# Kernel optimization log

Measured on AMD Instinct MI355X. Metric: run time of the kernel, lower is better.

The kernel has to match this reference:

```python
import jax, jax.numpy as jnp
import numpy as np

S = 64            # rendered_size
CLASS_NUM = 14    # dataset.enc_len
NEG_SLOPE = 0.01
EPS = 1e-5


def _conv(x, w, stride, pad):
    return jax.lax.conv_general_dilated(
        x, w, (stride, stride), [(pad, pad), (pad, pad)],
        dimension_numbers=("NCHW", "OIHW", "NCHW"))


def _bn(x, gamma, beta):
    # BatchNorm2d in training mode: biased batch stats over (N,H,W)
    m = jnp.mean(x, axis=(0, 2, 3), keepdims=True)
    v = jnp.var(x, axis=(0, 2, 3), keepdims=True)
    xn = (x - m) * jax.lax.rsqrt(v + EPS)
    return xn * gamma.reshape(1, -1, 1, 1) + beta.reshape(1, -1, 1, 1)


def _lrelu(x):
    return jnp.where(x >= 0, x, NEG_SLOPE * x)


def _render(elements):
    # elements: (B, N, class_num+4)
    rects = elements[:, :, -4:]
    cls = elements[:, :, :-4]                       # (B, N, C)
    x = rects[:, :, 0][:, :, None, None] * S        # (B, N, 1, 1)
    y = rects[:, :, 1][:, :, None, None] * S
    w = rects[:, :, 2][:, :, None, None] * S
    h = rects[:, :, 3][:, :, None, None] * S
    x0, x1 = x - 0.5 * w, x + 0.5 * w
    y0, y1 = y - 0.5 * h, y + 0.5 * h
    cx = jnp.arange(S, dtype=elements.dtype)[None, None, None, :]  # varies along W
    cy = jnp.arange(S, dtype=elements.dtype)[None, None, :, None]  # varies along H
    k = lambda c, cr: jnp.maximum(1.0 - jnp.abs(c - cr), 0.0)
    b0 = lambda c, cr: jnp.clip(c - cr, 0.0, 1.0)
    b1 = lambda cr, c: jnp.clip(cr - c, 0.0, 1.0)
    by = b0(cy, y0) * b1(y1, cy)                    # (B, N, S, S)
    bx = b0(cx, x0) * b1(x1, cx)
    l0 = k(cx, x0) * by
    l1 = k(cx, x1) * by
    l2 = k(cy, y0) * bx
    l3 = k(cy, y1) * bx
    rendered = jnp.maximum(jnp.maximum(l0, l1), jnp.maximum(l2, l3))  # (B,N,S,S)
    # sum over elements of class one-hot * rendered -> (B, C, S, S)
    return jnp.einsum("bnc,bnhw->bchw", cls, rendered)


def setup_inputs() -> dict:
    key = jax.random.key(0)
    ks = jax.random.split(key, 8)
    B, N = 64, 46
    inp = {
        "input_data": jax.random.uniform(ks[0], (B, N, CLASS_NUM + 4), dtype=jnp.float32),
        "input_length": jax.random.randint(ks[1], (B,), 0, N, dtype=jnp.int32),
        # cnn convs (bias=False) + BN affine params
        "w1": jax.random.normal(ks[2], (64, CLASS_NUM, 5, 5), jnp.float32) * 0.05,
        "g1": jnp.ones((64,), jnp.float32), "b1": jnp.zeros((64,), jnp.float32),
        "w2": jax.random.normal(ks[3], (128, 64, 5, 5), jnp.float32) * 0.03,
        "g2": jnp.ones((128,), jnp.float32), "b2": jnp.zeros((128,), jnp.float32),
        "w3": jax.random.normal(ks[4], (256, 128, 5, 5), jnp.float32) * 0.02,
        "g3": jnp.ones((256,), jnp.float32), "b3": jnp.zeros((256,), jnp.float32),
        # classifier: conv k=8 (bias=False) + BN + 1x1 conv (bias=True)
        "w4": jax.random.normal(ks[5], (1024, 256, 8, 8), jnp.float32) * 0.01,
        "g4": jnp.ones((1024,), jnp.float32), "b4": jnp.zeros((1024,), jnp.float32),
        "w5": jax.random.normal(ks[6], (1, 1024, 1, 1), jnp.float32) * 0.03,
        "b5": jnp.zeros((1,), jnp.float32),
    }
    return inp


def reference(input_data, input_length, w1, g1, b1, w2, g2, b2,
              w3, g3, b3, w4, g4, b4, w5, b5):
    rendered = _render(input_data)                       # (B, C, 64, 64)
    h = _lrelu(_bn(_conv(rendered, w1, 2, 2), g1, b1))   # (B, 64, 32, 32)
    h = _lrelu(_bn(_conv(h, w2, 2, 2), g2, b2))          # (B, 128, 16, 16)
    h = _lrelu(_bn(_conv(h, w3, 2, 2), g3, b3))          # (B, 256, 8, 8)
    h = _lrelu(_bn(_conv(h, w4, 1, 0), g4, b4))          # (B, 1024, 1, 1)
    out = _conv(h, w5, 1, 0) + b5.reshape(1, -1, 1, 1)   # (B, 1, 1, 1)
    return out.squeeze()                                 # (B,)
```

## Files before the change

### kernel.cpp

```cpp
#include <hip/hip_runtime.h>
#include <hip/hip_bf16.h>

#define NEG 0.01f
#define EPS 1e-5f

typedef __attribute__((ext_vector_type(8))) short short8;
typedef __attribute__((ext_vector_type(4))) float floatx4;

__device__ inline unsigned short f2bf(float f) {
    __hip_bfloat16 h = __float2bfloat16(f);
    union { __hip_bfloat16 h; unsigned short u; } cv; cv.h = h;
    return cv.u;
}

__global__ __launch_bounds__(256) void render_kernel(const float* __restrict__ in,
                                                     unsigned short* __restrict__ out) {
    int b = blockIdx.x >> 4;
    int chunk = blockIdx.x & 15;
    __shared__ float r0[46], r1[46], r2[46], r3[46];
    __shared__ float cls_s[46 * 14];
    int tid = threadIdx.x;
    if (tid < 46) {
        const float* p = in + ((size_t)b * 46 + tid) * 18 + 14;
        float x = p[0] * 64.f, y = p[1] * 64.f, w = p[2] * 64.f, h = p[3] * 64.f;
        r0[tid] = x - 0.5f * w; r1[tid] = x + 0.5f * w;
        r2[tid] = y - 0.5f * h; r3[tid] = y + 0.5f * h;
    }
    for (int idx = tid; idx < 46 * 14; idx += 256) {
        int n = idx / 14, c = idx % 14;
        cls_s[idx] = in[((size_t)b * 46 + n) * 18 + c];
    }
    __syncthreads();
    if (tid < 33) {
        int j = chunk * 33 + tid;
        if (j < 528) {
            int y, x;
            if (j < 136) { y = j / 68; x = j - y * 68; }
            else if (j < 272) { int t = j - 136; int yy = t / 68; y = 66 + yy; x = t - yy * 68; }
            else { int t = j - 272; y = 2 + (t >> 2); int k = t & 3; x = (k < 2) ? k : 64 + k; }
            size_t zb = (((size_t)b * 68 + y) * 68 + x) * 16;
            short8 z;
#pragma unroll
            for (int i = 0; i < 8; ++i) z[i] = 0;
            *(short8*)(out + zb) = z;
            *(short8*)(out + zb + 8) = z;
        }
    }
    int pix = chunk * 256 + tid;
    float cx = (float)(pix & 63);
    float cy = (float)(pix >> 6);
    float acc[14];
#pragma unroll
    for (int c = 0; c < 14; ++c) acc[c] = 0.f;
    for (int n = 0; n < 46; ++n) {
        float x0 = r0[n], x1 = r1[n], y0 = r2[n], y1 = r3[n];
        float by = fminf(fmaxf(cy - y0, 0.f), 1.f) * fminf(fmaxf(y1 - cy, 0.f), 1.f);
        float bx = fminf(fmaxf(cx - x0, 0.f), 1.f) * fminf(fmaxf(x1 - cx, 0.f), 1.f);
        float kx0 = fmaxf(1.f - fabsf(cx - x0), 0.f);
        float kx1 = fmaxf(1.f - fabsf(cx - x1), 0.f);
        float ky0 = fmaxf(1.f - fabsf(cy - y0), 0.f);
        float ky1 = fmaxf(1.f - fabsf(cy - y1), 0.f);
        float r = fmaxf(fmaxf(kx0 * by, kx1 * by), fmaxf(ky0 * bx, ky1 * bx));
        if (r > 0.f) {
#pragma unroll
            for (int c = 0; c < 14; ++c) acc[c] = fmaf(cls_s[n * 14 + c], r, acc[c]);
        }
    }
    size_t obase = (((size_t)b * 68 + ((pix >> 6) + 2)) * 68 + ((pix & 63) + 2)) * 16;
    short8 v0, v1;
#pragma unroll
    for (int i = 0; i < 8; ++i) v0[i] = (short)f2bf(acc[i]);
#pragma unroll
    for (int i = 0; i < 6; ++i) v1[i] = (short)f2bf(acc[8 + i]);
    v1[6] = 0; v1[7] = 0;
    *(short8*)(out + obase) = v0;
    *(short8*)(out + obase + 8) = v1;
}

__global__ __launch_bounds__(256) void wtrans_all(const float* __restrict__ w1,
                                                  const float* __restrict__ w2,
                                                  const float* __restrict__ w3,
                                                  unsigned short* __restrict__ wT1,
                                                  unsigned short* __restrict__ wT2,
                                                  unsigned short* __restrict__ wT3) {
    int idx = blockIdx.x * 256 + threadIdx.x;
    const float* w; unsigned short* wT; int CIN, CPLOG, SUB, COLOG;
    if (idx < 30720) { w = w1; wT = wT1; CIN = 14; CPLOG = 4; SUB = 3; COLOG = 6; }
    else if (idx < 235520) { idx -= 30720; w = w2; wT = wT2; CIN = 64; CPLOG = 6; SUB = 10; COLOG = 7; }
    else if (idx < 1054720) { idx -= 235520; w = w3; wT = wT3; CIN = 128; CPLOG = 7; SUB = 20; COLOG = 8; }
    else return;
    int kk = idx & 31;
    int co = (idx >> 5) & ((1 << COLOG) - 1);
    int s = idx >> (5 + COLOG);
    int kh = s / SUB, sub = s - kh * SUB;
    int kidx = sub * 32 + kk;
    int kw = kidx >> CPLOG;
    int ci = kidx & ((1 << CPLOG) - 1);
    float v = (kw < 5 && ci < CIN) ? w[((size_t)(co * CIN + ci) * 5 + kh) * 5 + kw] : 0.f;
    wT[idx] = f2bf(v);
}

template <int CP, int COUT, int HP, int LOG_OHW, int LOG_OW, int SUB,
          int NCO, int NT, int CH, int NW>
__global__ __launch_bounds__(NW * 64) void conv_mfma(
        const unsigned short* __restrict__ inP,
        const unsigned short* __restrict__ wT,
        float* __restrict__ outX,
        float* __restrict__ stacc) {
    constexpr int NSTEP = 5 * SUB;
    constexpr int NCHUNK = NSTEP / CH;
    constexpr int COT = NT * 16;
    constexpr int NSV = CH * COT * 4;
    constexpr int NSTG = (NSV + NW * 64 - 1) / (NW * 64);
    static_assert(NSTEP % CH == 0, "CH must divide NSTEP");
    __shared__ short Bs[2][CH][COT][32];
    __shared__ float sred[NW][2][COT];
    int tid = threadIdx.x;
    int wave = tid >> 6, lane = tid & 63, q = lane >> 4, l16 = lane & 15;
    int cpx = gridDim.x >> 3;
    int lb = (blockIdx.x & 7) * cpx + (blockIdx.x >> 3);
    int bm = lb / NCO, bco = lb % NCO;

    const short* aB[4];
#pragma unroll
    for (int f = 0; f < 4; ++f) {
        int m = bm * (NW * 64) + wave * 64 + f * 16 + l16;
        int b = m >> LOG_OHW;
        int ohw = m & ((1 << LOG_OHW) - 1);
        int oh = ohw >> LOG_OW, ow = ohw & ((1 << LOG_OW) - 1);
        aB[f] = (const short*)inP + ((size_t)((b * HP + 2 * oh) * HP + 2 * ow)) * CP + q * 8;
    }
    const short* bgbase = (const short*)wT + (size_t)bco * COT * 32;

    floatx4 acc[4][NT];
#pragma unroll
    for (int f = 0; f < 4; ++f)
#pragma unroll
        for (int nt = 0; nt < NT; ++nt) acc[f][nt] = (floatx4){0.f, 0.f, 0.f, 0.f};

    short8 nb[NSTG];
#pragma unroll
    for (int i = 0; i < NSTG; ++i) {
        int v = tid + i * NW * 64;
        if (v < NSV) {
            int s = v / (COT * 4);
            int rem = v - s * (COT * 4);
            nb[i] = *(const short8*)(bgbase + ((size_t)s * COUT) * 32 + rem * 8);
        }
    }
#pragma unroll
    for (int i = 0; i < NSTG; ++i) {
        int v = tid + i * NW * 64;
        if (v < NSV) {
            int s = v / (COT * 4);
            int rem = v - s * (COT * 4);
            *(short8*)((short*)&Bs[0][s][0][0] + rem * 8) = nb[i];
        }
    }
    short8 afc[4], afn[4];
#pragma unroll
    for (int f = 0; f < 4; ++f) afc[f] = *(const short8*)(aB[f]);
    __syncthreads();

    for (int chunk = 0; chunk < NCHUNK; ++chunk) {
        int cur = chunk & 1;
        if (chunk + 1 < NCHUNK) {
            int step0 = (chunk + 1) * CH;
#pragma unroll
            for (int i = 0; i < NSTG; ++i) {
                int v = tid + i * NW * 64;
                if (v < NSV) {
                    int s = v / (COT * 4);
                    int rem = v - s * (COT * 4);
                    nb[i] = *(const short8*)(bgbase + ((size_t)(step0 + s) * COUT) * 32 + rem * 8);
                }
            }
        }
#pragma unroll
        for (int s = 0; s < CH; ++s) {
            int step = chunk * CH + s;
            int stepn = step + 1;
            if (stepn < NSTEP) {
                int khn = stepn / SUB, subn = stepn - khn * SUB;
#pragma unroll
                for (int f = 0; f < 4; ++f)
                    afn[f] = *(const short8*)(aB[f] + (size_t)(khn * HP) * CP + subn * 32);
            }
#pragma unroll
            for (int nt = 0; nt < NT; ++nt) {
                short8 bf = *(const short8*)&Bs[cur][s][nt * 16 + l16][q * 8];
#pragma unroll
                for (int f = 0; f < 4; ++f)
                    acc[f][nt] = __builtin_amdgcn_mfma_f32_16x16x32_bf16(afc[f], bf, acc[f][nt], 0, 0, 0);
            }
#pragma unroll
            for (int f = 0; f < 4; ++f) afc[f] = afn[f];
        }
        if (chunk + 1 < NCHUNK) {
#pragma unroll
            for (int i = 0; i < NSTG; ++i) {
                int v = tid + i * NW * 64;
                if (v < NSV) {
                    int s = v / (COT * 4);
                    int rem = v - s * (COT * 4);
                    *(short8*)((short*)&Bs[cur ^ 1][s][0][0] + rem * 8) = nb[i];
                }
            }
            __syncthreads();
        }
    }
#pragma unroll
    for (int f = 0; f < 4; ++f)
#pragma unroll
        for (int nt = 0; nt < NT; ++nt)
#pragma unroll
            for (int rg = 0; rg < 4; ++rg) {
                int mg = bm * (NW * 64) + wave * 64 + f * 16 + q * 4 + rg;
                int co = bco * COT + nt * 16 + l16;
                outX[(size_t)mg * COUT + co] = acc[f][nt][rg];
            }
#pragma unroll
    for (int nt = 0; nt < NT; ++nt) {
        float s = 0.f, s2 = 0.f;
#pragma unroll
        for (int f = 0; f < 4; ++f)
#pragma unroll
            for (int rg = 0; rg < 4; ++rg) {
                float v = acc[f][nt][rg];
                s += v; s2 = fmaf(v, v, s2);
            }
        s += __shfl_xor(s, 16); s += __shfl_xor(s, 32);
        s2 += __shfl_xor(s2, 16); s2 += __shfl_xor(s2, 32);
        if (q == 0) {
            sred[wave][0][nt * 16 + l16] = s;
            sred[wave][1][nt * 16 + l16] = s2;
        }
    }
    __syncthreads();
    if (tid < COT) {
        float ts = 0.f, ts2 = 0.f;
#pragma unroll
        for (int w = 0; w < NW; ++w) { ts += sred[w][0][tid]; ts2 += sred[w][1][tid]; }
        atomicAdd(&stacc[bco * COT + tid], ts);
        atomicAdd(&stacc[COUT + bco * COT + tid], ts2);
    }
}

__global__ __launch_bounds__(256) void conv4_mfma(const unsigned short* __restrict__ A,
                                                  const float* __restrict__ w4,
                                                  float* __restrict__ h4) {
    constexpr int CH = 4, NCHUNK = 8;
    __shared__ short Bs[CH][64][40];
    int tid = threadIdx.x;
    int bco = blockIdx.x & 15;
    int ks = blockIdx.x >> 4;
    int wave = tid >> 6, lane = tid & 63, q = lane >> 4, l16 = lane & 15;
    const short* aBase = (const short*)A + (size_t)(wave * 16 + l16) * 16384 + ks * 1024 + q * 8;
    int r = tid >> 2, cc = tid & 3;
    const float* bg = w4 + (size_t)(bco * 64 + r) * 16384 + ks * 1024 + cc * 8;

    floatx4 acc[4];
#pragma unroll
    for (int nt = 0; nt < 4; ++nt) acc[nt] = (floatx4){0.f, 0.f, 0.f, 0.f};

    short8 nb[CH];
#pragma unroll
    for (int s = 0; s < CH; ++s) {
        float4 b0 = *(const float4*)(bg + s * 32);
        float4 b1 = *(const float4*)(bg + s * 32 + 4);
        nb[s][0] = (short)f2bf(b0.x); nb[s][1] = (short)f2bf(b0.y);
        nb[s][2] = (short)f2bf(b0.z); nb[s][3] = (short)f2bf(b0.w);
        nb[s][4] = (short)f2bf(b1.x); nb[s][5] = (short)f2bf(b1.y);
        nb[s][6] = (short)f2bf(b1.z); nb[s][7] = (short)f2bf(b1.w);
    }
#pragma unroll
    for (int s = 0; s < CH; ++s) *(short8*)&Bs[s][r][cc * 8] = nb[s];
    __syncthreads();

    for (int chunk = 0; chunk < NCHUNK; ++chunk) {
        bool has_next = (chunk + 1 < NCHUNK);
        if (has_next) {
#pragma unroll
            for (int s = 0; s < CH; ++s) {
                int step = (chunk + 1) * CH + s;
                float4 b0 = *(const float4*)(bg + step * 32);
                float4 b1 = *(const float4*)(bg + step * 32 + 4);
                nb[s][0] = (short)f2bf(b0.x); nb[s][1] = (short)f2bf(b0.y);
                nb[s][2] = (short)f2bf(b0.z); nb[s][3] = (short)f2bf(b0.w);
                nb[s][4] = (short)f2bf(b1.x); nb[s][5] = (short)f2bf(b1.y);
                nb[s][6] = (short)f2bf(b1.z); nb[s][7] = (short)f2bf(b1.w);
            }
        }
#pragma unroll
        for (int s = 0; s < CH; ++s) {
            int step = chunk * CH + s;
            short8 af = *(const short8*)(aBase + step * 32);
#pragma unroll
            for (int nt = 0; nt < 4; ++nt) {
                short8 bf = *(const short8*)&Bs[s][nt * 16 + l16][q * 8];
                acc[nt] = __builtin_amdgcn_mfma_f32_16x16x32_bf16(af, bf, acc[nt], 0, 0, 0);
            }
        }
        if (has_next) {
            __syncthreads();
#pragma unroll
            for (int s = 0; s < CH; ++s) *(short8*)&Bs[s][r][cc * 8] = nb[s];
            __syncthreads();
        }
    }
#pragma unroll
    for (int nt = 0; nt < 4; ++nt) {
#pragma unroll
        for (int rg = 0; rg < 4; ++rg) {
            int mg = wave * 16 + q * 4 + rg;
            int co = bco * 64 + nt * 16 + l16;
            atomicAdd(&h4[(size_t)mg * 1024 + co], acc[nt][rg]);
        }
    }
}

__global__ __launch_bounds__(256) void stats_part(const float* __restrict__ X,
                                                  float* __restrict__ acc,
                                                  int CO, int R, int RPB, int CGLOG) {
    int tid = threadIdx.x;
    int cg = blockIdx.x & ((1 << CGLOG) - 1);
    int rb = blockIdx.x >> CGLOG;
    int c = (cg << 6) + (tid & 63);
    int w = tid >> 6;
    float s = 0.f, s2 = 0.f;
    int rend = min(R, (rb + 1) * RPB);
    for (int r = rb * RPB + w; r < rend; r += 4) {
        float v = X[(size_t)r * CO + c];
        s += v; s2 += v * v;
    }
    __shared__ float ls[4][64], ls2[4][64];
    ls[w][tid & 63] = s; ls2[w][tid & 63] = s2;
    __syncthreads();
    if (tid < 64) {
        float ts = ls[0][tid] + ls[1][tid] + ls[2][tid] + ls[3][tid];
        float ts2 = ls2[0][tid] + ls2[1][tid] + ls2[2][tid] + ls2[3][tid];
        int cc = (cg << 6) + tid;
        atomicAdd(&acc[cc], ts);
        atomicAdd(&acc[CO + cc], ts2);
    }
}

__global__ __launch_bounds__(256) void bnpad_kernel(const float* __restrict__ X,
                                                    const float* __restrict__ stacc,
                                                    const float* __restrict__ g,
                                                    const float* __restrict__ bb,
                                                    unsigned short* __restrict__ out,
                                                    int CO_LOG, int OH, int OHP,
                                                    float invN, int total) {
    int idx = blockIdx.x * 256 + threadIdx.x;
    if (idx >= total) return;
    int CO = 1 << CO_LOG;
    int c = idx & (CO - 1);
    float mean = stacc[c] * invN;
    float var = fmaxf(stacc[CO + c] * invN - mean * mean, 0.f);
    float sc = g[c] * rsqrtf(var + EPS);
    float sh = bb[c] - mean * sc;
    int t = idx >> CO_LOG;
    int x = t % OHP; t /= OHP;
    int y = t % OHP; int b = t / OHP;
    unsigned short v = 0;
    if (y >= 2 && y < OH + 2 && x >= 2 && x < OH + 2) {
        float f = X[(((size_t)(b * OH + (y - 2)) * OH + (x - 2)) << CO_LOG) + c];
        f = f * sc + sh;
        f = f >= 0.f ? f : NEG * f;
        v = f2bf(f);
    }
    out[idx] = v;
}

__global__ __launch_bounds__(256) void bn_nchw_kernel(const float* __restrict__ X,
                                                      const float* __restrict__ stacc,
                                                      const float* __restrict__ g,
                                                      const float* __restrict__ bb,
                                                      unsigned short* __restrict__ out,
                                                      int total) {
    int idx = blockIdx.x * 256 + threadIdx.x;
    if (idx >= total) return;
    int hw = idx & 63;
    int ci = (idx >> 6) & 255;
    int b = idx >> 14;
    float mean = stacc[ci] * (1.f / 4096.f);
    float var = fmaxf(stacc[256 + ci] * (1.f / 4096.f) - mean * mean, 0.f);
    float sc = g[ci] * rsqrtf(var + EPS);
    float sh = bb[ci] - mean * sc;
    float f = X[((size_t)(b * 64 + hw)) * 256 + ci] * sc + sh;
    f = f >= 0.f ? f : NEG * f;
    out[idx] = f2bf(f);
}

__global__ __launch_bounds__(256) void conv5_kernel(const float* __restrict__ X,
                                                    const float* __restrict__ stacc,
                                                    const float* __restrict__ g,
                                                    const float* __restrict__ bb,
                                                    const float* __restrict__ w5,
                                                    const float* __restrict__ b5,
                                                    float* __restrict__ out) {
    int b = blockIdx.x, tid = threadIdx.x;
    float s = 0.f;
    for (int c = tid; c < 1024; c += 256) {
        float mean = stacc[c] * (1.f / 64.f);
        float var = fmaxf(stacc[1024 + c] * (1.f / 64.f) - mean * mean, 0.f);
        float sc = g[c] * rsqrtf(var + EPS);
        float sh = bb[c] - mean * sc;
        float f = X[(size_t)b * 1024 + c] * sc + sh;
        f = f >= 0.f ? f : NEG * f;
        s = fmaf(f, w5[c], s);
    }
#pragma unroll
    for (int off = 32; off > 0; off >>= 1) s += __shfl_down(s, off);
    __shared__ float ls[4];
    if ((tid & 63) == 0) ls[tid >> 6] = s;
    __syncthreads();
    if (tid == 0) out[b] = ls[0] + ls[1] + ls[2] + ls[3] + b5[0];
}

extern "C" void kernel_launch(void* const* d_in, const int* in_sizes, int n_in,
                              void* d_out, int out_size, void* d_ws, size_t ws_size,
                              hipStream_t stream) {
    (void)in_sizes; (void)n_in; (void)out_size; (void)ws_size;
    const float* input_data = (const float*)d_in[0];
    const float* w1 = (const float*)d_in[2];
    const float* g1 = (const float*)d_in[3];
    const float* b1 = (const float*)d_in[4];
    const float* w2 = (const float*)d_in[5];
    const float* g2 = (const float*)d_in[6];
    const float* b2 = (const float*)d_in[7];
    const float* w3 = (const float*)d_in[8];
    const float* g3 = (const float*)d_in[9];
    const float* b3 = (const float*)d_in[10];
    const float* w4 = (const float*)d_in[11];
    const float* g4 = (const float*)d_in[12];
    const float* b4 = (const float*)d_in[13];
    const float* w5 = (const float*)d_in[14];
    const float* b5 = (const float*)d_in[15];

    char* ws = (char*)d_ws;
    float* regA = (float*)ws;
    char* wsB = ws + 16777216;
    char* wsC = wsB + 10616832;
    char* wsD = wsC + 9469952;
    float* h4  = (float*)wsD;
    float* st1 = (float*)(wsD + 262144);
    float* st2 = (float*)(wsD + 262656);
    float* st3 = (float*)(wsD + 263680);
    float* st4 = (float*)(wsD + 265728);
    unsigned short* wT1 = (unsigned short*)(wsD + 274432);
    unsigned short* wT2 = (unsigned short*)(wsD + 335872);
    unsigned short* wT3 = (unsigned short*)(wsD + 745472);

    unsigned short* rendered = (unsigned short*)wsC;
    float* conv1out = regA;
    unsigned short* pad1 = (unsigned short*)wsB;
    float* conv2out = (float*)wsC;
    unsigned short* pad2 = (unsigned short*)wsB;
    float* conv3out = regA;
    unsigned short* a4 = (unsigned short*)wsC;

    hipMemsetAsync(wsD, 0, 273920, stream);
    wtrans_all<<<4120, 256, 0, stream>>>(w1, w2, w3, wT1, wT2, wT3);
    render_kernel<<<1024, 256, 0, stream>>>(input_data, rendered);

    conv_mfma<16, 64, 68, 10, 5, 3, 1, 4, 5, 4><<<256, 256, 0, stream>>>(rendered, wT1, conv1out, st1);
    bnpad_kernel<<<20736, 256, 0, stream>>>(conv1out, st1, g1, b1, pad1, 6, 32, 36, 1.f / 65536.f, 5308416);

    conv_mfma<64, 128, 36, 8, 4, 10, 4, 2, 10, 4><<<256, 256, 0, stream>>>(pad1, wT2, conv2out, st2);
    bnpad_kernel<<<12800, 256, 0, stream>>>(conv2out, st2, g2, b2, pad2, 7, 16, 20, 1.f / 16384.f, 3276800);

    conv_mfma<128, 256, 20, 6, 3, 20, 8, 2, 10, 2><<<256, 128, 0, stream>>>(pad2, wT3, conv3out, st3);
    bn_nchw_kernel<<<4096, 256, 0, stream>>>(conv3out, st3, g3, b3, a4, 1048576);

    conv4_mfma<<<256, 256, 0, stream>>>(a4, w4, h4);
    stats_part<<<16, 256, 0, stream>>>(h4, st4, 1024, 64, 64, 4);

    conv5_kernel<<<64, 256, 0, stream>>>(h4, st4, g4, b4, w5, b5, (float*)d_out);
}
```

Before: 277.1 us.

## Split-K conv2 and conv3 with atomic accumulation and separate stats pass

Adds a KSEG template parameter so conv2 and conv3 split their reduction dimension across 2 and 5 blocks, raising grid sizes from 256 to 512 and 1280 blocks. Partial results are combined with atomicAdd into zeroed fp32 buffers, which moves to a dedicated workspace region and needs a much larger memset. Because no single block sees the full sum, BN statistics are no longer fused into the conv epilogue, so a separate stats_part pass reads the output again. The aim is better CU occupancy on the small-grid layers, paid for with atomic traffic, a larger memset and an extra reduction kernel.

```diff
diff --git a/kernel.cpp b/kernel.cpp
--- a/kernel.cpp
+++ b/kernel.cpp
@@ -101,17 +101,19 @@
 }
 
 template <int CP, int COUT, int HP, int LOG_OHW, int LOG_OW, int SUB,
-          int NCO, int NT, int CH, int NW>
+          int NCO, int NT, int CH, int NW, int KSEG>
 __global__ __launch_bounds__(NW * 64) void conv_mfma(
         const unsigned short* __restrict__ inP,
         const unsigned short* __restrict__ wT,
         float* __restrict__ outX,
         float* __restrict__ stacc) {
-    constexpr int NSTEP = 5 * SUB;
+    constexpr int NSTEP_TOT = 5 * SUB;
+    constexpr int NSTEP = NSTEP_TOT / KSEG;
     constexpr int NCHUNK = NSTEP / CH;
     constexpr int COT = NT * 16;
     constexpr int NSV = CH * COT * 4;
     constexpr int NSTG = (NSV + NW * 64 - 1) / (NW * 64);
+    static_assert(NSTEP_TOT % KSEG == 0, "KSEG must divide total steps");
     static_assert(NSTEP % CH == 0, "CH must divide NSTEP");
     __shared__ short Bs[2][CH][COT][32];
     __shared__ float sred[NW][2][COT];
@@ -119,7 +121,11 @@
     int wave = tid >> 6, lane = tid & 63, q = lane >> 4, l16 = lane & 15;
     int cpx = gridDim.x >> 3;
     int lb = (blockIdx.x & 7) * cpx + (blockIdx.x >> 3);
-    int bm = lb / NCO, bco = lb % NCO;
+    int bm = lb / (NCO * KSEG);
+    int rem = lb - bm * (NCO * KSEG);
+    int bco = rem / KSEG;
+    int kseg = rem - bco * KSEG;
+    int kbase = kseg * NSTEP;
 
     const short* aB[4];
 #pragma unroll
@@ -144,8 +150,8 @@
         int v = tid + i * NW * 64;
         if (v < NSV) {
             int s = v / (COT * 4);
-            int rem = v - s * (COT * 4);
-            nb[i] = *(const short8*)(bgbase + ((size_t)s * COUT) * 32 + rem * 8);
+            int rem2 = v - s * (COT * 4);
+            nb[i] = *(const short8*)(bgbase + ((size_t)(kbase + s) * COUT) * 32 + rem2 * 8);
         }
     }
 #pragma unroll
@@ -153,35 +159,39 @@
         int v = tid + i * NW * 64;
         if (v < NSV) {
             int s = v / (COT * 4);
-            int rem = v - s * (COT * 4);
-            *(short8*)((short*)&Bs[0][s][0][0] + rem * 8) = nb[i];
+            int rem2 = v - s * (COT * 4);
+            *(short8*)((short*)&Bs[0][s][0][0] + rem2 * 8) = nb[i];
         }
     }
     short8 afc[4], afn[4];
-#pragma unroll
-    for (int f = 0; f < 4; ++f) afc[f] = *(const short8*)(aB[f]);
+    {
+        int kh0 = kbase / SUB, sub0 = kbase - kh0 * SUB;
+#pragma unroll
+        for (int f = 0; f < 4; ++f)
+            afc[f] = *(const short8*)(aB[f] + (size_t)(kh0 * HP) * CP + sub0 * 32);
+    }
     __syncthreads();
 
     for (int chunk = 0; chunk < NCHUNK; ++chunk) {
         int cur = chunk & 1;
         if (chunk + 1 < NCHUNK) {
-            int step0 = (chunk + 1) * CH;
+            int step0 = kbase + (chunk + 1) * CH;
 #pragma unroll
             for (int i = 0; i < NSTG; ++i) {
                 int v = tid + i * NW * 64;
                 if (v < NSV) {
                     int s = v / (COT * 4);
-                    int rem = v - s * (COT * 4);
-                    nb[i] = *(const short8*)(bgbase + ((size_t)(step0 + s) * COUT) * 32 + rem * 8);
+                    int rem2 = v - s * (COT * 4);
+                    nb[i] = *(const short8*)(bgbase + ((size_t)(step0 + s) * COUT) * 32 + rem2 * 8);
                 }
             }
         }
 #pragma unroll
         for (int s = 0; s < CH; ++s) {
-            int step = chunk * CH + s;
-            int stepn = step + 1;
-            if (stepn < NSTEP) {
-                int khn = stepn / SUB, subn = stepn - khn * SUB;
+            int lstep = chunk * CH + s;
+            if (lstep + 1 < NSTEP) {
+                int gsn = kbase + lstep + 1;
+                int khn = gsn / SUB, subn = gsn - khn * SUB;
 #pragma unroll
                 for (int f = 0; f < 4; ++f)
                     afn[f] = *(const short8*)(aB[f] + (size_t)(khn * HP) * CP + subn * 32);
@@ -202,8 +212,8 @@
                 int v = tid + i * NW * 64;
                 if (v < NSV) {
                     int s = v / (COT * 4);
-                    int rem = v - s * (COT * 4);
-                    *(short8*)((short*)&Bs[cur ^ 1][s][0][0] + rem * 8) = nb[i];
+                    int rem2 = v - s * (COT * 4);
+                    *(short8*)((short*)&Bs[cur ^ 1][s][0][0] + rem2 * 8) = nb[i];
                 }
             }
             __syncthreads();
@@ -217,32 +227,37 @@
             for (int rg = 0; rg < 4; ++rg) {
                 int mg = bm * (NW * 64) + wave * 64 + f * 16 + q * 4 + rg;
                 int co = bco * COT + nt * 16 + l16;
-                outX[(size_t)mg * COUT + co] = acc[f][nt][rg];
-            }
-#pragma unroll
-    for (int nt = 0; nt < NT; ++nt) {
-        float s = 0.f, s2 = 0.f;
-#pragma unroll
-        for (int f = 0; f < 4; ++f)
-#pragma unroll
-            for (int rg = 0; rg < 4; ++rg) {
-                float v = acc[f][nt][rg];
-                s += v; s2 = fmaf(v, v, s2);
-            }
-        s += __shfl_xor(s, 16); s += __shfl_xor(s, 32);
-        s2 += __shfl_xor(s2, 16); s2 += __shfl_xor(s2, 32);
-        if (q == 0) {
-            sred[wave][0][nt * 16 + l16] = s;
-            sred[wave][1][nt * 16 + l16] = s2;
-        }
-    }
-    __syncthreads();
-    if (tid < COT) {
-        float ts = 0.f, ts2 = 0.f;
-#pragma unroll
-        for (int w = 0; w < NW; ++w) { ts += sred[w][0][tid]; ts2 += sred[w][1][tid]; }
-        atomicAdd(&stacc[bco * COT + tid], ts);
-        atomicAdd(&stacc[COUT + bco * COT + tid], ts2);
+                if constexpr (KSEG > 1)
+                    atomicAdd(&outX[(size_t)mg * COUT + co], acc[f][nt][rg]);
+                else
+                    outX[(size_t)mg * COUT + co] = acc[f][nt][rg];
+            }
+    if constexpr (KSEG == 1) {
+#pragma unroll
+        for (int nt = 0; nt < NT; ++nt) {
+            float s = 0.f, s2 = 0.f;
+#pragma unroll
+            for (int f = 0; f < 4; ++f)
+#pragma unroll
+                for (int rg = 0; rg < 4; ++rg) {
+                    float v = acc[f][nt][rg];
+                    s += v; s2 = fmaf(v, v, s2);
+                }
+            s += __shfl_xor(s, 16); s += __shfl_xor(s, 32);
+            s2 += __shfl_xor(s2, 16); s2 += __shfl_xor(s2, 32);
+            if (q == 0) {
+                sred[wave][0][nt * 16 + l16] = s;
+                sred[wave][1][nt * 16 + l16] = s2;
+            }
+        }
+        __syncthreads();
+        if (tid < COT) {
+            float ts = 0.f, ts2 = 0.f;
+#pragma unroll
+            for (int w = 0; w < NW; ++w) { ts += sred[w][0][tid]; ts2 += sred[w][1][tid]; }
+            atomicAdd(&stacc[bco * COT + tid], ts);
+            atomicAdd(&stacc[COUT + bco * COT + tid], ts2);
+        }
     }
 }
 
@@ -449,29 +464,31 @@
     float* st2 = (float*)(wsD + 262656);
     float* st3 = (float*)(wsD + 263680);
     float* st4 = (float*)(wsD + 265728);
-    unsigned short* wT1 = (unsigned short*)(wsD + 274432);
-    unsigned short* wT2 = (unsigned short*)(wsD + 335872);
-    unsigned short* wT3 = (unsigned short*)(wsD + 745472);
+    float* conv2out = (float*)(wsD + 273920);
+    float* conv3out = (float*)(wsD + 8662528);
+    unsigned short* wT1 = (unsigned short*)(wsD + 12856832);
+    unsigned short* wT2 = (unsigned short*)(wsD + 12918272);
+    unsigned short* wT3 = (unsigned short*)(wsD + 13327872);
 
     unsigned short* rendered = (unsigned short*)wsC;
     float* conv1out = regA;
     unsigned short* pad1 = (unsigned short*)wsB;
-    float* conv2out = (float*)wsC;
     unsigned short* pad2 = (unsigned short*)wsB;
-    float* conv3out = regA;
     unsigned short* a4 = (unsigned short*)wsC;
 
-    hipMemsetAsync(wsD, 0, 273920, stream);
+    hipMemsetAsync(wsD, 0, 12856832, stream);
     wtrans_all<<<4120, 256, 0, stream>>>(w1, w2, w3, wT1, wT2, wT3);
     render_kernel<<<1024, 256, 0, stream>>>(input_data, rendered);
 
-    conv_mfma<16, 64, 68, 10, 5, 3, 1, 4, 5, 4><<<256, 256, 0, stream>>>(rendered, wT1, conv1out, st1);
+    conv_mfma<16, 64, 68, 10, 5, 3, 1, 4, 5, 4, 1><<<256, 256, 0, stream>>>(rendered, wT1, conv1out, st1);
     bnpad_kernel<<<20736, 256, 0, stream>>>(conv1out, st1, g1, b1, pad1, 6, 32, 36, 1.f / 65536.f, 5308416);
 
-    conv_mfma<64, 128, 36, 8, 4, 10, 4, 2, 10, 4><<<256, 256, 0, stream>>>(pad1, wT2, conv2out, st2);
+    conv_mfma<64, 128, 36, 8, 4, 10, 4, 2, 5, 4, 2><<<512, 256, 0, stream>>>(pad1, wT2, conv2out, st2);
+    stats_part<<<256, 256, 0, stream>>>(conv2out, st2, 128, 16384, 128, 1);
     bnpad_kernel<<<12800, 256, 0, stream>>>(conv2out, st2, g2, b2, pad2, 7, 16, 20, 1.f / 16384.f, 3276800);
 
-    conv_mfma<128, 256, 20, 6, 3, 20, 8, 2, 10, 2><<<256, 128, 0, stream>>>(pad2, wT3, conv3out, st3);
+    conv_mfma<128, 256, 20, 6, 3, 20, 8, 2, 5, 2, 5><<<1280, 128, 0, stream>>>(pad2, wT3, conv3out, st3);
+    stats_part<<<256, 256, 0, stream>>>(conv3out, st3, 256, 4096, 64, 2);
     bn_nchw_kernel<<<4096, 256, 0, stream>>>(conv3out, st3, g3, b3, a4, 1048576);
 
     conv4_mfma<<<256, 256, 0, stream>>>(a4, w4, h4);
```

New measurement: 306.7 us. +10.7%, slower.
